# Kernel tuning notes

Measured on AMD Instinct MI355X. Metric: run time of the kernel, lower is better.

The kernel has to match this reference:

```python
import jax, jax.numpy as jnp
import numpy as np
from jax import lax

DIM = 256
HEADS = 8
DIM_HEAD = 32
INNER = HEADS * DIM_HEAD  # 256
SCALE = DIM_HEAD ** -0.5
EPS = 1e-5
DN = ('NCHW', 'OIHW', 'NCHW')


def chan_layer_norm(x, g):
    # LayerNorm over channel dim (axis=1), biased variance
    mean = jnp.mean(x, axis=1, keepdims=True)
    var = jnp.mean((x - mean) ** 2, axis=1, keepdims=True)
    return (x - mean) / jnp.sqrt(var + EPS) * g


def conv1x1(x, w):
    return lax.conv_general_dilated(x, w, (1, 1), 'VALID', dimension_numbers=DN)


def dwconv3x3(x, w):
    # depthwise 3x3, padding=1, groups=channels; w: [C,1,3,3]
    return lax.conv_general_dilated(x, w, (1, 1), 'SAME', dimension_numbers=DN,
                                    feature_group_count=x.shape[1])


def setup_inputs() -> dict:
    key = jax.random.key(0)
    ks = jax.random.split(key, 9)
    B, X, Y = 16, 64, 64
    fmap = jax.random.normal(ks[0], (B, DIM, X, Y), dtype=jnp.float32)
    w = lambda k, shape: (jax.random.normal(k, shape, dtype=jnp.float32) * 0.02)
    return {
        'fmap': fmap,
        'g_norm': jnp.ones((1, DIM, 1, 1), dtype=jnp.float32),
        'wq1': w(ks[1], (INNER, DIM, 1, 1)),
        'wq_dw': w(ks[2], (INNER, 1, 3, 3)),
        'wk1': w(ks[3], (INNER, DIM, 1, 1)),
        'wk_dw': w(ks[4], (INNER, 1, 3, 3)),
        'wv1': w(ks[5], (INNER, DIM, 1, 1)),
        'wv_dw': w(ks[6], (INNER, 1, 3, 3)),
        'wo': w(ks[7], (DIM, INNER, 1, 1)),
        'g_out': jnp.ones((1, DIM, 1, 1), dtype=jnp.float32),
    }


def reference(fmap, g_norm, wq1, wq_dw, wk1, wk_dw, wv1, wv_dw, wo, g_out):
    b, _, X, Y = fmap.shape
    n = X * Y
    x = chan_layer_norm(fmap, g_norm)
    # QKV: 1x1 conv -> depthwise 3x3 conv (dropout is identity in eval)
    q = dwconv3x3(conv1x1(x, wq1), wq_dw)
    k = dwconv3x3(conv1x1(x, wk1), wk_dw)
    v = dwconv3x3(conv1x1(x, wv1), wv_dw)
    # b (h c) x y -> b h n c
    def split(t):
        return t.reshape(b, HEADS, DIM_HEAD, n).transpose(0, 1, 3, 2)
    q, k, v = split(q), split(k), split(v)
    q = jax.nn.softmax(q, axis=-1) * SCALE   # softmax over feature dim
    k = jax.nn.softmax(k, axis=-2)           # softmax over sequence dim
    ctx = jnp.einsum('bhnd,bhne->bhde', k, v)    # [b,h,d,d]
    out = jnp.einsum('bhnd,bhde->bhne', q, ctx)  # [b,h,n,d]
    # b h n d -> b (h d) x y
    out = out.transpose(0, 1, 3, 2).reshape(b, INNER, X, Y)
    out = jax.nn.silu(out)
    out = conv1x1(out, wo)
    return chan_layer_norm(out, g_out)
```

## Files before the change

### kernel.cpp

```cpp
#include <hip/hip_runtime.h>


typedef unsigned short u16;
typedef __bf16 bf16x8 __attribute__((ext_vector_type(8)));
typedef float f32x4 __attribute__((ext_vector_type(4)));
typedef float f32x16 __attribute__((ext_vector_type(16)));

#define DEV static __device__ __forceinline__

DEV float b2f(u16 u) { return __uint_as_float(((unsigned int)u) << 16); }
DEV u16 f2bf(float f) {
  unsigned int u = __float_as_uint(f);
  return (u16)((u + 0x7fffu + ((u >> 16) & 1u)) >> 16);
}
DEV void gl2lds16(const void* g, void* l) {
  __builtin_amdgcn_global_load_lds((__attribute__((address_space(1))) void*)g,
                                   (__attribute__((address_space(3))) void*)l, 16, 0, 0);
}

__global__ __launch_bounds__(256) void prep_kernel(const float* __restrict__ wk,
                                                   const float* __restrict__ wv,
                                                   const float* __restrict__ wq,
                                                   const float* __restrict__ wo,
                                                   u16* __restrict__ wb) {
  const int i = blockIdx.x * 256 + threadIdx.x;
  const int yb = blockIdx.y;
  if (yb == 0)      wb[(i >> 8) * 512 + (i & 255)] = f2bf(wk[i]);
  else if (yb == 1) wb[(i >> 8) * 512 + 256 + (i & 255)] = f2bf(wv[i]);
  else if (yb == 2) wb[131072 + i] = f2bf(wq[i]);
  else              wb[196608 + i] = f2bf(wo[i]);
}

__global__ __launch_bounds__(256) void ln_tin_kernel(const float* __restrict__ f,
                                                     const float* __restrict__ g,
                                                     u16* __restrict__ xT) {
  __shared__ u16 tile[64 * 268];
  __shared__ float red[2 * 256];
  __shared__ float mu_s[64], inv_s[64];
  const int t = threadIdx.x;
  const int p0 = blockIdx.x * 64;
  const int b = blockIdx.y;
  const long fb = (long)b * 256 * 4096;
  const int p = t & 63, cg = t >> 6;
  float s1 = 0.f, s2 = 0.f;
  for (int pass = 0; pass < 64; ++pass) {
    int c = pass * 4 + cg;
    float v = f[fb + (long)c * 4096 + p0 + p];
    s1 += v; s2 += v * v;
    tile[p * 268 + c] = f2bf(v);
  }
  red[cg * 64 + p] = s1;
  red[256 + cg * 64 + p] = s2;
  __syncthreads();
  if (t < 64) {
    float a1 = red[t] + red[64 + t] + red[128 + t] + red[192 + t];
    float a2 = red[256 + t] + red[320 + t] + red[384 + t] + red[448 + t];
    float mu = a1 * (1.f / 256.f);
    float var = a2 * (1.f / 256.f) - mu * mu;
    mu_s[t] = mu;
    inv_s[t] = 1.0f / sqrtf(var + 1e-5f);
  }
  __syncthreads();
  {
    const int ch8 = (t & 31) * 8, wp = t >> 5;
    float ga[8];
#pragma unroll
    for (int e = 0; e < 8; ++e) ga[e] = g[ch8 + e];
#pragma unroll
    for (int pass = 0; pass < 8; ++pass) {
      const int px = pass * 8 + wp;
      uint2 lo = *(const uint2*)&tile[px * 268 + ch8];
      uint2 hi = *(const uint2*)&tile[px * 268 + ch8 + 4];
      const u16* sl = (const u16*)&lo;
      const u16* sh = (const u16*)&hi;
      const float mu = mu_s[px], inv = inv_s[px];
      uint4 o;
      u16* os = (u16*)&o;
#pragma unroll
      for (int e = 0; e < 4; ++e) os[e] = f2bf((b2f(sl[e]) - mu) * inv * ga[e]);
#pragma unroll
      for (int e = 0; e < 4; ++e) os[4 + e] = f2bf((b2f(sh[e]) - mu) * inv * ga[4 + e]);
      *(uint4*)&xT[((long)b * 4096 + p0 + px) * 256 + ch8] = o;
    }
  }
}

__global__ __launch_bounds__(256) void gemm_bt_kernel(
    const u16* __restrict__ A, const u16* __restrict__ B0, const u16* __restrict__ B1,
    u16* __restrict__ Cg, int ldc, long sA, long sC) {
  __shared__ u16 As[128 * 32];
  __shared__ u16 Bs[128 * 32];
  const int t = threadIdx.x;
  const int wave = t >> 6, lane = t & 63, quad = lane >> 4, l16 = lane & 15;
  const int wr = wave >> 1, wc = wave & 1;
  const int m0 = blockIdx.x * 128;
  const int jt = blockIdx.y;
  const int b = blockIdx.z;
  const u16* Ab = A + (long)b * sA + (long)m0 * 256;
  const u16* Bt = (jt < 2 ? B0 : B1) + (jt & 1) * 128 * 256;
  u16* Cb = Cg + (long)b * sC + (long)m0 * ldc + jt * 128;

  const int srow = lane >> 2;
  const int scol = (lane & 3) * 8;
  f32x4 acc[4][4];
#pragma unroll
  for (int i = 0; i < 4; ++i)
#pragma unroll
    for (int j = 0; j < 4; ++j) acc[i][j] = (f32x4){0.f, 0.f, 0.f, 0.f};

  const int aoff = (wr * 64 + l16) * 32 + quad * 8;
  const int boff = (wc * 64 + l16) * 32 + quad * 8;

  for (int ks = 0; ks < 8; ++ks) {
    const int k0 = ks * 32;
    __syncthreads();
    for (int i = wave; i < 8; i += 4) {
      gl2lds16(Ab + (i * 16 + srow) * 256 + k0 + scol, &As[i * 512 + lane * 8]);
      gl2lds16(Bt + (i * 16 + srow) * 256 + k0 + scol, &Bs[i * 512 + lane * 8]);
    }
    __syncthreads();
    bf16x8 af[4], bfr[4];
#pragma unroll
    for (int mt = 0; mt < 4; ++mt) af[mt] = *(const bf16x8*)&As[aoff + mt * 512];
#pragma unroll
    for (int nt = 0; nt < 4; ++nt) bfr[nt] = *(const bf16x8*)&Bs[boff + nt * 512];
#pragma unroll
    for (int mt = 0; mt < 4; ++mt)
#pragma unroll
      for (int nt = 0; nt < 4; ++nt)
        acc[mt][nt] = __builtin_amdgcn_mfma_f32_16x16x32_bf16(af[mt], bfr[nt], acc[mt][nt], 0, 0, 0);
  }
#pragma unroll
  for (int mt = 0; mt < 4; ++mt) {
    const int mbase = wr * 64 + mt * 16 + quad * 4;
#pragma unroll
    for (int nt = 0; nt < 4; ++nt) {
      const int n = wc * 64 + nt * 16 + l16;
#pragma unroll
      for (int r = 0; r < 4; ++r)
        Cb[(long)(mbase + r) * ldc + n] = f2bf(acc[mt][nt][r]);
    }
  }
}

__global__ __launch_bounds__(256) void dwq_kernel(const u16* __restrict__ qT,
                                                  const float* __restrict__ wdw,
                                                  u16* __restrict__ qp) {
  __shared__ u16 tile[6 * 66 * 40];
  const int t = threadIdx.x;
  const int strip = blockIdx.x, h = blockIdx.y, b = blockIdx.z;
  const int x0 = strip * 4;
  const int wave = t >> 6, lane = t & 63;
  const int ysel = lane & 15, cg = lane >> 4;
  const int y = wave * 16 + ysel;
  const int ty = t >> 2, tc = t & 3;

  if (t < 48) {
    const int slot = t >> 3, brd = (t >> 2) & 1, c4 = t & 3;
    *(uint4*)&tile[slot * 2640 + (brd ? 65 * 40 : 0) + c4 * 8] = (uint4){0, 0, 0, 0};
  }
  const u16* qrow = qT + (long)b * 4096 * 256 + h * 32 + tc * 8;
#pragma unroll
  for (int s = 0; s < 6; ++s) {
    const int xx = x0 - 1 + s;
    uint4 v = (uint4){0, 0, 0, 0};
    if ((unsigned)xx < 64u) v = *(const uint4*)(qrow + (long)(xx * 64 + ty) * 256);
    *(uint4*)&tile[s * 2640 + (ty + 1) * 40 + tc * 8] = v;
  }
  float w[72];
#pragma unroll
  for (int q = 0; q < 8; ++q)
#pragma unroll
    for (int i = 0; i < 9; ++i) w[q * 9 + i] = wdw[(h * 32 + cg * 8 + q) * 9 + i];
  __syncthreads();

  u16* ob = qp + ((long)b * 4096 + y) * 256 + h * 32 + cg * 8;
#pragma unroll
  for (int it = 0; it < 4; ++it) {
    const int x = x0 + it;
    float acc[8] = {0.f, 0.f, 0.f, 0.f, 0.f, 0.f, 0.f, 0.f};
#pragma unroll
    for (int r = 0; r < 3; ++r) {
#pragma unroll
      for (int dy = 0; dy < 3; ++dy) {
        uint4 pk = *(const uint4*)&tile[(it + r) * 2640 + (y + dy) * 40 + cg * 8];
        const u16* s = (const u16*)&pk;
#pragma unroll
        for (int q = 0; q < 8; ++q)
          acc[q] = fmaf(w[q * 9 + r * 3 + dy], b2f(s[q]), acc[q]);
      }
    }
    float e[8];
    float s = 0.f;
#pragma unroll
    for (int q = 0; q < 8; ++q) { e[q] = __expf(acc[q]); s += e[q]; }
    s += __shfl_xor(s, 16);
    s += __shfl_xor(s, 32);
    const float inv = 0.17677669529663687f / s;
    uint4 o;
    u16* os = (u16*)&o;
#pragma unroll
    for (int q = 0; q < 8; ++q) os[q] = f2bf(e[q] * inv);
    *(uint4*)(ob + (long)x * 16384) = o;
  }
}

__global__ __launch_bounds__(1024, 4) void ctx_kernel(const u16* __restrict__ kvT,
                                                      const float* __restrict__ wkdw,
                                                      const float* __restrict__ wvdw,
                                                      float* __restrict__ par0,
                                                      float* __restrict__ par1) {
  __shared__ float redb[8 * 1088];
  __shared__ float redk[16 * 32];
  const int t = threadIdx.x;
  const int strip = blockIdx.x, h = blockIdx.y, b = blockIdx.z;
  const int wave = t >> 6, lane = t & 63;
  const int g = wave >> 2, wq = wave & 3;
  const int x0 = strip * 32 + g * 8;
  const int c = lane & 31, half = lane >> 5;
  const int ystart = wq * 16 + half * 8;
  float wk[9], wv[9];
#pragma unroll
  for (int i = 0; i < 9; ++i) {
    wk[i] = wkdw[(h * 32 + c) * 9 + i];
    wv[i] = wvdw[(h * 32 + c) * 9 + i];
  }
  const u16* kb = kvT + (long)b * 4096 * 512 + 2 * (h * 32 + c);

  float fk[3][10], fv[3][10];
  unsigned pk[10];
#pragma unroll
  for (int r = 0; r < 2; ++r) {
    const int x = x0 - 1 + r;
#pragma unroll
    for (int m = 0; m < 10; ++m) {
      const int yy = ystart - 1 + m;
      float a = 0.f, bb = 0.f;
      if (((unsigned)x < 64u) & ((unsigned)yy < 64u)) {
        const unsigned u = *(const unsigned*)(kb + (long)(x * 64 + yy) * 512);
        a = b2f((u16)(u & 0xffffu));
        bb = b2f((u16)(u >> 16));
      }
      fk[r][m] = a; fv[r][m] = bb;
    }
  }
#pragma unroll
  for (int m = 0; m < 10; ++m) {
    const int yy = ystart - 1 + m;
    unsigned u = 0;
    if (((unsigned)(x0 + 1) < 64u) & ((unsigned)yy < 64u))
      u = *(const unsigned*)(kb + (long)((x0 + 1) * 64 + yy) * 512);
    pk[m] = u;
  }
#pragma unroll
  for (int m = 0; m < 10; ++m) {
    fk[2][m] = __uint_as_float(pk[m] << 16);
    fv[2][m] = __uint_as_float(pk[m] & 0xffff0000u);
  }
  f32x16 acc;
#pragma unroll
  for (int r = 0; r < 16; ++r) acc[r] = 0.f;
  float ks = 0.f;

  for (int it = 0; it < 8; ++it) {
    const int xn = x0 + it + 2;
#pragma unroll
    for (int m = 0; m < 10; ++m) {
      const int yy = ystart - 1 + m;
      unsigned u = 0;
      if (((unsigned)xn < 64u) & ((unsigned)yy < 64u))
        u = *(const unsigned*)(kb + (long)(xn * 64 + yy) * 512);
      pk[m] = u;
    }
    union { bf16x8 v; u16 s[8]; } af, bf_;
#pragma unroll
    for (int j = 0; j < 8; ++j) {
      float a = 0.f, bb = 0.f;
#pragma unroll
      for (int r = 0; r < 3; ++r)
#pragma unroll
        for (int dy = 0; dy < 3; ++dy) {
          a = fmaf(wk[r * 3 + dy], fk[r][j + dy], a);
          bb = fmaf(wv[r * 3 + dy], fv[r][j + dy], bb);
        }
      const u16 eb = f2bf(__expf(a));
      ks += b2f(eb);
      af.s[j] = eb;
      bf_.s[j] = f2bf(bb);
    }
    acc = __builtin_amdgcn_mfma_f32_32x32x16_bf16(af.v, bf_.v, acc, 0, 0, 0);
#pragma unroll
    for (int m = 0; m < 10; ++m) {
      fk[0][m] = fk[1][m]; fv[0][m] = fv[1][m];
      fk[1][m] = fk[2][m]; fv[1][m] = fv[2][m];
      fk[2][m] = __uint_as_float(pk[m] << 16);
      fv[2][m] = __uint_as_float(pk[m] & 0xffff0000u);
    }
  }
  ks += __shfl_xor(ks, 32);
  if (half == 0) redk[wave * 32 + c] = ks;
  if (wave >= 8) {
#pragma unroll
    for (int r = 0; r < 16; ++r) redb[(wave - 8) * 1088 + lane * 17 + r] = acc[r];
  }
  __syncthreads();
  if (wave < 8) {
#pragma unroll
    for (int r = 0; r < 16; ++r) acc[r] += redb[wave * 1088 + lane * 17 + r];
  }
  __syncthreads();
  if (wave >= 4 && wave < 8) {
#pragma unroll
    for (int r = 0; r < 16; ++r) redb[(wave - 4) * 1088 + lane * 17 + r] = acc[r];
  }
  __syncthreads();
  if (wave < 4) {
#pragma unroll
    for (int r = 0; r < 16; ++r) acc[r] += redb[wave * 1088 + lane * 17 + r];
  }
  __syncthreads();
  if (wave >= 1 && wave < 4) {
#pragma unroll
    for (int r = 0; r < 16; ++r) redb[(wave - 1) * 1088 + lane * 17 + r] = acc[r];
  }
  __syncthreads();
  if (wave == 0) {
    float* par = (strip ? par1 : par0) + (long)(b * 8 + h) * 1056;
#pragma unroll
    for (int r = 0; r < 16; ++r) {
      float sum = acc[r] + redb[lane * 17 + r] + redb[1088 + lane * 17 + r] +
                  redb[2176 + lane * 17 + r];
      const int d = (r & 3) + 8 * (r >> 2) + 4 * half;
      par[d * 32 + c] = sum;
    }
    if (t < 32) {
      float s = 0.f;
#pragma unroll
      for (int w = 0; w < 16; ++w) s += redk[w * 32 + t];
      par[1024 + t] = s;
    }
  }
}

__global__ __launch_bounds__(256) void attn_kernel(const u16* __restrict__ qp,
                                                   const float* __restrict__ par0,
                                                   const float* __restrict__ par1,
                                                   u16* __restrict__ sout) {
  __shared__ u16 cnhi[2 * 32 * 40];
  __shared__ u16 cnlo[2 * 32 * 40];
  const int t = threadIdx.x;
  const int p0 = blockIdx.x * 128;
  const int hp = blockIdx.y;
  const int b = blockIdx.z;
  const int wave = t >> 6, lane = t & 63, quad = lane >> 4, l16 = lane & 15;

  for (int j = 0; j < 8; ++j) {
    const int lidx = j * 256 + t;
    const int e = lidx & 31, d = (lidx >> 5) & 31, hh = lidx >> 10;
    const long base = (long)(b * 8 + hp * 2 + hh) * 1056;
    const float ks = par0[base + 1024 + d] + par1[base + 1024 + d];
    const float c = (par0[base + d * 32 + e] + par1[base + d * 32 + e]) / ks;
    const u16 hi = f2bf(c);
    cnhi[hh * 1280 + e * 40 + d] = hi;
    cnlo[hh * 1280 + e * 40 + d] = f2bf(c - b2f(hi));
  }
  __syncthreads();

  const u16* qb = qp + ((long)b * 4096 + p0 + wave * 32) * 256;
  u16* ob = sout + ((long)b * 4096 + p0 + wave * 32) * 256;
#pragma unroll
  for (int hh = 0; hh < 2; ++hh) {
    const int h = hp * 2 + hh;
    const int cb = hh * 1280 + quad * 8;
    const bf16x8 bhi0 = *(const bf16x8*)&cnhi[cb + l16 * 40];
    const bf16x8 bhi1 = *(const bf16x8*)&cnhi[cb + (16 + l16) * 40];
    const bf16x8 blo0 = *(const bf16x8*)&cnlo[cb + l16 * 40];
    const bf16x8 blo1 = *(const bf16x8*)&cnlo[cb + (16 + l16) * 40];
#pragma unroll
    for (int rt = 0; rt < 2; ++rt) {
      const bf16x8 af = *(const bf16x8*)&qb[(rt * 16 + l16) * 256 + h * 32 + quad * 8];
      f32x4 a0 = (f32x4){0.f, 0.f, 0.f, 0.f};
      f32x4 a1 = (f32x4){0.f, 0.f, 0.f, 0.f};
      a0 = __builtin_amdgcn_mfma_f32_16x16x32_bf16(af, blo0, a0, 0, 0, 0);
      a0 = __builtin_amdgcn_mfma_f32_16x16x32_bf16(af, bhi0, a0, 0, 0, 0);
      a1 = __builtin_amdgcn_mfma_f32_16x16x32_bf16(af, blo1, a1, 0, 0, 0);
      a1 = __builtin_amdgcn_mfma_f32_16x16x32_bf16(af, bhi1, a1, 0, 0, 0);
#pragma unroll
      for (int r = 0; r < 4; ++r) {
        const int row = rt * 16 + quad * 4 + r;
        const float v0 = a0[r], v1 = a1[r];
        ob[(long)row * 256 + h * 32 + l16] = f2bf(v0 / (1.f + __expf(-v0)));
        ob[(long)row * 256 + h * 32 + 16 + l16] = f2bf(v1 / (1.f + __expf(-v1)));
      }
    }
  }
}

__global__ __launch_bounds__(256) void ln_tout_kernel(const u16* __restrict__ y,
                                                      const float* __restrict__ gout,
                                                      float* __restrict__ out) {
  __shared__ u16 tile[64 * 268];
  __shared__ float red[2 * 256];
  __shared__ float mu_s[64], inv_s[64];
  const int t = threadIdx.x;
  const int p0 = blockIdx.x * 64;
  const int b = blockIdx.y;
  {
    const int px = t >> 2, q = t & 3;
    const u16* yrow = y + ((long)b * 4096 + p0 + px) * 256;
    float s1 = 0.f, s2 = 0.f;
#pragma unroll
    for (int j = 0; j < 8; ++j) {
      const int ch = q * 8 + j * 32;
      uint4 v = *(const uint4*)&yrow[ch];
      const u16* s = (const u16*)&v;
#pragma unroll
      for (int e = 0; e < 8; ++e) {
        float fv = b2f(s[e]);
        s1 += fv; s2 += fv * fv;
      }
      *(uint2*)&tile[px * 268 + ch] = (uint2){v.x, v.y};
      *(uint2*)&tile[px * 268 + ch + 4] = (uint2){v.z, v.w};
    }
    red[q * 64 + px] = s1;
    red[256 + q * 64 + px] = s2;
  }
  __syncthreads();
  if (t < 64) {
    float s1 = red[t] + red[64 + t] + red[128 + t] + red[192 + t];
    float s2 = red[256 + t] + red[320 + t] + red[384 + t] + red[448 + t];
    float mu = s1 * (1.f / 256.f);
    float var = s2 * (1.f / 256.f) - mu * mu;
    mu_s[t] = mu;
    inv_s[t] = 1.0f / sqrtf(var + 1e-5f);
  }
  __syncthreads();
  {
    const int lpx = t & 63, cw = t >> 6;
    const long ob = (long)b * 256 * 4096;
    const float mu = mu_s[lpx], inv = inv_s[lpx];
#pragma unroll
    for (int pass = 0; pass < 16; ++pass) {
      const int c4 = pass * 16 + cw * 4;
      uint2 v = *(const uint2*)&tile[lpx * 268 + c4];
      const u16* s = (const u16*)&v;
#pragma unroll
      for (int i = 0; i < 4; ++i)
        out[ob + (long)(c4 + i) * 4096 + p0 + lpx] = (b2f(s[i]) - mu) * inv * gout[c4 + i];
    }
  }
}

extern "C" void kernel_launch(void* const* d_in, const int* in_sizes, int n_in,
                              void* d_out, int out_size, void* d_ws, size_t ws_size,
                              hipStream_t stream) {
  (void)in_sizes; (void)n_in; (void)out_size; (void)ws_size;
  const float* fmap = (const float*)d_in[0];
  const float* gnorm = (const float*)d_in[1];
  const float* wq1 = (const float*)d_in[2];
  const float* wqdw = (const float*)d_in[3];
  const float* wk1 = (const float*)d_in[4];
  const float* wkdw = (const float*)d_in[5];
  const float* wv1 = (const float*)d_in[6];
  const float* wvdw = (const float*)d_in[7];
  const float* wo = (const float*)d_in[8];
  const float* gout = (const float*)d_in[9];
  float* out = (float*)d_out;
  char* ws = (char*)d_ws;

  float* par0 = (float*)(ws);
  u16* wb = (u16*)(ws + 540672);
  float* par1 = (float*)(ws + 1064960);
  u16* wkv_bf = wb;
  u16* wq_bf = wb + 131072;
  u16* wo_bf = wb + 196608;
  u16* xT = (u16*)(ws + 2097152);
  u16* kvT = (u16*)(ws + 35651584);
  u16* qT = kvT;
  u16* qp = (u16*)(ws + 69206016);
  u16* sbuf = xT;
  u16* ybuf = qp;

  prep_kernel<<<dim3(256, 4), 256, 0, stream>>>(wk1, wv1, wq1, wo, wb);
  ln_tin_kernel<<<dim3(64, 16), 256, 0, stream>>>(fmap, gnorm, xT);
  gemm_bt_kernel<<<dim3(32, 4, 16), 256, 0, stream>>>(xT, wkv_bf, wkv_bf + 65536, kvT, 512,
                                                      4096L * 256, 4096L * 512);
  ctx_kernel<<<dim3(2, 8, 16), 1024, 0, stream>>>(kvT, wkdw, wvdw, par0, par1);
  gemm_bt_kernel<<<dim3(32, 2, 16), 256, 0, stream>>>(xT, wq_bf, wq_bf, qT, 256,
                                                      4096L * 256, 4096L * 256);
  dwq_kernel<<<dim3(16, 8, 16), 256, 0, stream>>>(qT, wqdw, qp);
  attn_kernel<<<dim3(32, 4, 16), 256, 0, stream>>>(qp, par0, par1, sbuf);
  gemm_bt_kernel<<<dim3(32, 2, 16), 256, 0, stream>>>(sbuf, wo_bf, wo_bf, ybuf, 256,
                                                      4096L * 256, 4096L * 256);
  ln_tout_kernel<<<dim3(64, 16), 256, 0, stream>>>(ybuf, gout, out);
}
```

Baseline: 304.2 us.

## Fuse attention apply, output projection and output LayerNorm into one kernel

Merges the attention-context multiply with SiLU, the Wo 1x1 GEMM and the final channel LayerNorm into a single kernel that processes 64 pixels across all 8 heads. The SiLU output and projected tile stay in LDS instead of round-tripping through global memory, and two kernel launches go away. In exchange, each block rebuilds the full 8-head context matrices, reads Wo B-fragments directly from global memory, and uses about 77KB of LDS. That limits occupancy and launches only 1024 blocks.

```diff
diff --git a/kernel.cpp b/kernel.cpp
--- a/kernel.cpp
+++ b/kernel.cpp
@@ -342,43 +342,48 @@
   }
 }
 
-__global__ __launch_bounds__(256) void attn_kernel(const u16* __restrict__ qp,
-                                                   const float* __restrict__ par0,
-                                                   const float* __restrict__ par1,
-                                                   u16* __restrict__ sout) {
-  __shared__ u16 cnhi[2 * 32 * 40];
-  __shared__ u16 cnlo[2 * 32 * 40];
+__global__ __launch_bounds__(256) void attn_o_ln_kernel(const u16* __restrict__ qp,
+                                                        const float* __restrict__ par0,
+                                                        const float* __restrict__ par1,
+                                                        const u16* __restrict__ wo_bf,
+                                                        const float* __restrict__ gout,
+                                                        float* __restrict__ out) {
+  __shared__ char smem[77312];
+  u16* cnhi = (u16*)smem;
+  u16* cnlo = (u16*)(smem + 20480);
+  u16* ytile = (u16*)smem;
+  u16* stile = (u16*)(smem + 40960);
+  float* red = (float*)(smem + 74752);
+  float* mu_s = (float*)(smem + 76800);
+  float* inv_s = (float*)(smem + 77056);
   const int t = threadIdx.x;
-  const int p0 = blockIdx.x * 128;
-  const int hp = blockIdx.y;
+  const int p0 = blockIdx.x * 64;
   const int b = blockIdx.z;
   const int wave = t >> 6, lane = t & 63, quad = lane >> 4, l16 = lane & 15;
 
-  for (int j = 0; j < 8; ++j) {
+  for (int j = 0; j < 32; ++j) {
     const int lidx = j * 256 + t;
-    const int e = lidx & 31, d = (lidx >> 5) & 31, hh = lidx >> 10;
-    const long base = (long)(b * 8 + hp * 2 + hh) * 1056;
+    const int e = lidx & 31, d = (lidx >> 5) & 31, h = lidx >> 10;
+    const long base = (long)(b * 8 + h) * 1056;
     const float ks = par0[base + 1024 + d] + par1[base + 1024 + d];
     const float c = (par0[base + d * 32 + e] + par1[base + d * 32 + e]) / ks;
     const u16 hi = f2bf(c);
-    cnhi[hh * 1280 + e * 40 + d] = hi;
-    cnlo[hh * 1280 + e * 40 + d] = f2bf(c - b2f(hi));
-  }
-  __syncthreads();
-
-  const u16* qb = qp + ((long)b * 4096 + p0 + wave * 32) * 256;
-  u16* ob = sout + ((long)b * 4096 + p0 + wave * 32) * 256;
-#pragma unroll
-  for (int hh = 0; hh < 2; ++hh) {
-    const int h = hp * 2 + hh;
-    const int cb = hh * 1280 + quad * 8;
-    const bf16x8 bhi0 = *(const bf16x8*)&cnhi[cb + l16 * 40];
-    const bf16x8 bhi1 = *(const bf16x8*)&cnhi[cb + (16 + l16) * 40];
-    const bf16x8 blo0 = *(const bf16x8*)&cnlo[cb + l16 * 40];
-    const bf16x8 blo1 = *(const bf16x8*)&cnlo[cb + (16 + l16) * 40];
-#pragma unroll
-    for (int rt = 0; rt < 2; ++rt) {
-      const bf16x8 af = *(const bf16x8*)&qb[(rt * 16 + l16) * 256 + h * 32 + quad * 8];
+    cnhi[h * 1280 + e * 40 + d] = hi;
+    cnlo[h * 1280 + e * 40 + d] = f2bf(c - b2f(hi));
+  }
+  __syncthreads();
+
+  {
+    const u16* qb = qp + ((long)b * 4096 + p0 + wave * 16) * 256;
+    const int srow = wave * 16 + quad * 4;
+#pragma unroll
+    for (int h = 0; h < 8; ++h) {
+      const int cb = h * 1280 + quad * 8;
+      const bf16x8 bhi0 = *(const bf16x8*)&cnhi[cb + l16 * 40];
+      const bf16x8 bhi1 = *(const bf16x8*)&cnhi[cb + (16 + l16) * 40];
+      const bf16x8 blo0 = *(const bf16x8*)&cnlo[cb + l16 * 40];
+      const bf16x8 blo1 = *(const bf16x8*)&cnlo[cb + (16 + l16) * 40];
+      const bf16x8 af = *(const bf16x8*)&qb[l16 * 256 + h * 32 + quad * 8];
       f32x4 a0 = (f32x4){0.f, 0.f, 0.f, 0.f};
       f32x4 a1 = (f32x4){0.f, 0.f, 0.f, 0.f};
       a0 = __builtin_amdgcn_mfma_f32_16x16x32_bf16(af, blo0, a0, 0, 0, 0);
@@ -387,40 +392,65 @@
       a1 = __builtin_amdgcn_mfma_f32_16x16x32_bf16(af, bhi1, a1, 0, 0, 0);
 #pragma unroll
       for (int r = 0; r < 4; ++r) {
-        const int row = rt * 16 + quad * 4 + r;
+        const int row = srow + r;
         const float v0 = a0[r], v1 = a1[r];
-        ob[(long)row * 256 + h * 32 + l16] = f2bf(v0 / (1.f + __expf(-v0)));
-        ob[(long)row * 256 + h * 32 + 16 + l16] = f2bf(v1 / (1.f + __expf(-v1)));
+        stile[row * 264 + h * 32 + l16] = f2bf(v0 / (1.f + __expf(-v0)));
+        stile[row * 264 + h * 32 + 16 + l16] = f2bf(v1 / (1.f + __expf(-v1)));
       }
     }
   }
-}
-
-__global__ __launch_bounds__(256) void ln_tout_kernel(const u16* __restrict__ y,
-                                                      const float* __restrict__ gout,
-                                                      float* __restrict__ out) {
-  __shared__ u16 tile[64 * 268];
-  __shared__ float red[2 * 256];
-  __shared__ float mu_s[64], inv_s[64];
-  const int t = threadIdx.x;
-  const int p0 = blockIdx.x * 64;
-  const int b = blockIdx.y;
+  __syncthreads();
+
+  {
+    const int n0 = wave * 64;
+    f32x4 acc[4][4];
+#pragma unroll
+    for (int i = 0; i < 4; ++i)
+#pragma unroll
+      for (int j = 0; j < 4; ++j) acc[i][j] = (f32x4){0.f, 0.f, 0.f, 0.f};
+#pragma unroll
+    for (int ks = 0; ks < 8; ++ks) {
+      const int k0 = ks * 32;
+      bf16x8 af[4], bfr[4];
+#pragma unroll
+      for (int mt = 0; mt < 4; ++mt)
+        af[mt] = *(const bf16x8*)&stile[(mt * 16 + l16) * 264 + k0 + quad * 8];
+#pragma unroll
+      for (int nt = 0; nt < 4; ++nt)
+        bfr[nt] = *(const bf16x8*)&wo_bf[(n0 + nt * 16 + l16) * 256 + k0 + quad * 8];
+#pragma unroll
+      for (int mt = 0; mt < 4; ++mt)
+#pragma unroll
+        for (int nt = 0; nt < 4; ++nt)
+          acc[mt][nt] = __builtin_amdgcn_mfma_f32_16x16x32_bf16(af[mt], bfr[nt], acc[mt][nt], 0, 0, 0);
+    }
+#pragma unroll
+    for (int mt = 0; mt < 4; ++mt) {
+      const int rb = mt * 16 + quad * 4;
+#pragma unroll
+      for (int nt = 0; nt < 4; ++nt) {
+        const int col = n0 + nt * 16 + l16;
+#pragma unroll
+        for (int r = 0; r < 4; ++r)
+          ytile[(rb + r) * 264 + col] = f2bf(acc[mt][nt][r]);
+      }
+    }
+  }
+  __syncthreads();
+
   {
     const int px = t >> 2, q = t & 3;
-    const u16* yrow = y + ((long)b * 4096 + p0 + px) * 256;
     float s1 = 0.f, s2 = 0.f;
 #pragma unroll
     for (int j = 0; j < 8; ++j) {
       const int ch = q * 8 + j * 32;
-      uint4 v = *(const uint4*)&yrow[ch];
+      uint4 v = *(const uint4*)&ytile[px * 264 + ch];
       const u16* s = (const u16*)&v;
 #pragma unroll
       for (int e = 0; e < 8; ++e) {
         float fv = b2f(s[e]);
         s1 += fv; s2 += fv * fv;
       }
-      *(uint2*)&tile[px * 268 + ch] = (uint2){v.x, v.y};
-      *(uint2*)&tile[px * 268 + ch + 4] = (uint2){v.z, v.w};
     }
     red[q * 64 + px] = s1;
     red[256 + q * 64 + px] = s2;
@@ -442,7 +472,7 @@
 #pragma unroll
     for (int pass = 0; pass < 16; ++pass) {
       const int c4 = pass * 16 + cw * 4;
-      uint2 v = *(const uint2*)&tile[lpx * 268 + c4];
+      uint2 v = *(const uint2*)&ytile[lpx * 264 + c4];
       const u16* s = (const u16*)&v;
 #pragma unroll
       for (int i = 0; i < 4; ++i)
@@ -478,8 +508,6 @@
   u16* kvT = (u16*)(ws + 35651584);
   u16* qT = kvT;
   u16* qp = (u16*)(ws + 69206016);
-  u16* sbuf = xT;
-  u16* ybuf = qp;
 
   prep_kernel<<<dim3(256, 4), 256, 0, stream>>>(wk1, wv1, wq1, wo, wb);
   ln_tin_kernel<<<dim3(64, 16), 256, 0, stream>>>(fmap, gnorm, xT);
@@ -489,8 +517,5 @@
   gemm_bt_kernel<<<dim3(32, 2, 16), 256, 0, stream>>>(xT, wq_bf, wq_bf, qT, 256,
                                                       4096L * 256, 4096L * 256);
   dwq_kernel<<<dim3(16, 8, 16), 256, 0, stream>>>(qT, wqdw, qp);
-  attn_kernel<<<dim3(32, 4, 16), 256, 0, stream>>>(qp, par0, par1, sbuf);
-  gemm_bt_kernel<<<dim3(32, 2, 16), 256, 0, stream>>>(sbuf, wo_bf, wo_bf, ybuf, 256,
-                                                      4096L * 256, 4096L * 256);
-  ln_tout_kernel<<<dim3(64, 16), 256, 0, stream>>>(ybuf, gout, out);
-}
+  attn_o_ln_kernel<<<dim3(64, 1, 16), 256, 0, stream>>>(qp, par0, par1, wo_bf, gout, out);
+}
```

Measured after the change: 307.2 us. About the same (+1.0%).
